# Kernel tuning notes

Hardware: AMD Instinct MI355X
Metric: run time of the kernel (lower is better)

The kernel has to match this reference:

```python
import jax, jax.numpy as jnp
import numpy as np

B, S, D = 4, 2048, 1024
H, DH = 16, 64


def setup_inputs() -> dict:
    key = jax.random.key(0)
    ks = jax.random.split(key, 5)
    x = jax.random.normal(ks[0], (B, S, D), dtype=jnp.float32)
    # causal mask: True where attention is disallowed (j > i)
    mask = jnp.triu(jnp.ones((S, S), dtype=bool), k=1)
    mask = jnp.broadcast_to(mask, (B, S, S))
    scale = 1.0 / np.sqrt(D)
    w_q = jax.random.normal(ks[1], (D, D), dtype=jnp.float32) * scale
    w_k = jax.random.normal(ks[2], (D, D), dtype=jnp.float32) * scale
    w_v = jax.random.normal(ks[3], (D, D), dtype=jnp.float32) * scale
    w_o = jax.random.normal(ks[4], (D, D), dtype=jnp.float32) * scale
    return {"x": x, "mask": mask, "w_q": w_q, "w_k": w_k, "w_v": w_v, "w_o": w_o}


def reference(x, mask, w_q, w_k, w_v, w_o):
    # torch Linear: y = x @ W.T (bias=False)
    b, s, d = x.shape
    q = (x @ w_q.T).reshape(b, s, H, DH).transpose(0, 2, 1, 3)  # [B,H,S,DH]
    k = (x @ w_k.T).reshape(b, s, H, DH).transpose(0, 2, 1, 3)
    v = (x @ w_v.T).reshape(b, s, H, DH).transpose(0, 2, 1, 3)
    inv_sqrt_dh = jnp.asarray(1.0 / np.sqrt(DH), dtype=x.dtype)
    scores = jnp.einsum('bhqd,bhkd->bhqk', q * inv_sqrt_dh, k)  # [B,H,S,S]
    scores = jnp.where(mask[:, None, :, :], -jnp.inf, scores)
    attn = jax.nn.softmax(scores, axis=-1)  # dropout is identity in eval mode
    out = jnp.einsum('bhqk,bhkd->bhqd', attn, v)  # [B,H,S,DH]
    out = out.transpose(0, 2, 1, 3).reshape(b, s, d)
    out = out @ w_o.T
    return out, attn
```

## Files before the change

kernel.cpp:

```cpp
#include <hip/hip_runtime.h>

#define DEV __device__ __forceinline__

typedef __attribute__((ext_vector_type(8))) short short8;
typedef __attribute__((ext_vector_type(4))) float f32x4;

DEV unsigned short f2bf(float f) {
  unsigned u = __builtin_bit_cast(unsigned, f);
  u += 0x7fff + ((u >> 16) & 1);
  return (unsigned short)(u >> 16);
}

DEV void gload_lds16(const void* g, void* l) {
  __builtin_amdgcn_global_load_lds(
      (const __attribute__((address_space(1))) void*)g,
      (__attribute__((address_space(3))) void*)l, 16, 0, 0);
}

#if __has_builtin(__builtin_amdgcn_exp2f)
#define EXP2F(x) __builtin_amdgcn_exp2f(x)
#else
#define EXP2F(x) exp2f(x)
#endif

#define LOG2E 1.4426950408889634f
#define QSCALE (0.125f * LOG2E)
#define MFMA16(a, b, c) __builtin_amdgcn_mfma_f32_16x16x32_bf16((a), (b), (c), 0, 0, 0)

__global__ void cvt_f32_bf16(const float* __restrict__ in, unsigned short* __restrict__ out, int n4) {
  int i = blockIdx.x * blockDim.x + threadIdx.x;
  int stride = gridDim.x * blockDim.x;
  for (; i < n4; i += stride) {
    float4 v = ((const float4*)in)[i];
    ushort4 o;
    o.x = f2bf(v.x); o.y = f2bf(v.y); o.z = f2bf(v.z); o.w = f2bf(v.w);
    ((ushort4*)out)[i] = o;
  }
}

__global__ void cvt_w4(const float* __restrict__ w0, const float* __restrict__ w1,
                       const float* __restrict__ w2, const float* __restrict__ w3,
                       unsigned short* __restrict__ o0, unsigned short* __restrict__ o1,
                       unsigned short* __restrict__ o2, unsigned short* __restrict__ o3) {
  int i = blockIdx.x * blockDim.x + threadIdx.x;
  int sel = i >> 18, j = i & 0x3ffff;
  const float* in = sel == 0 ? w0 : sel == 1 ? w1 : sel == 2 ? w2 : w3;
  unsigned short* out = sel == 0 ? o0 : sel == 1 ? o1 : sel == 2 ? o2 : o3;
  float4 v = ((const float4*)in)[j];
  ushort4 o;
  o.x = f2bf(v.x); o.y = f2bf(v.y); o.z = f2bf(v.z); o.w = f2bf(v.w);
  ((ushort4*)out)[j] = o;
}

#define GK 1024
template <int MODE>
DEV void gemm_body(const unsigned short* A, const unsigned short* Bw, void* Cout,
                   int bx, int by) {
  __shared__ unsigned short Ash[128 * 32];
  __shared__ unsigned short Bsh[128 * 32];
  const int tid = threadIdx.x;
  const int lane = tid & 63;
  const int w = tid >> 6;
  const int wm = w >> 1, wn = w & 1;
  const int l15 = lane & 15, l4 = lane >> 4;
  const int row0 = by * 128;
  const int col0 = bx * 128;

  f32x4 acc[4][4] = {};

  for (int kt = 0; kt < GK; kt += 32) {
    __syncthreads();
#pragma unroll
    for (int c = 0; c < 2; ++c) {
      int o = c * 4096 + tid * 16;
      int ldsoff = c * 4096 + w * 1024;
      int row = o >> 6, colb = o & 63;
      gload_lds16((const char*)A + (size_t)(row0 + row) * 2048 + kt * 2 + colb,
                  (char*)Ash + ldsoff);
      gload_lds16((const char*)Bw + (size_t)(col0 + row) * 2048 + kt * 2 + colb,
                  (char*)Bsh + ldsoff);
    }
    __syncthreads();
    short8 af[4], bf[4];
#pragma unroll
    for (int m = 0; m < 4; ++m)
      af[m] = *(const short8*)((const char*)Ash + (wm * 64 + m * 16 + l15) * 64 + l4 * 16);
#pragma unroll
    for (int n = 0; n < 4; ++n)
      bf[n] = *(const short8*)((const char*)Bsh + (wn * 64 + n * 16 + l15) * 64 + l4 * 16);
#pragma unroll
    for (int m = 0; m < 4; ++m)
#pragma unroll
      for (int n = 0; n < 4; ++n)
        acc[m][n] = MFMA16(af[m], bf[n], acc[m][n]);
  }

#pragma unroll
  for (int m = 0; m < 4; ++m)
#pragma unroll
    for (int n = 0; n < 4; ++n)
#pragma unroll
      for (int r = 0; r < 4; ++r) {
        int mrow = row0 + wm * 64 + m * 16 + l4 * 4 + r;
        int ncol = col0 + wn * 64 + n * 16 + l15;
        float v = acc[m][n][r];
        if (MODE == 0) {
          ((unsigned short*)Cout)[(size_t)mrow * 1024 + ncol] = f2bf(v);
        } else if (MODE == 1) {
          int b = mrow >> 11, s = mrow & 2047, h = ncol >> 6, d = ncol & 63;
          ((unsigned short*)Cout)[((size_t)((b * 16 + h) * 64 + d)) * 2048 + s] = f2bf(v);
        } else if (MODE == 2) {
          ((float*)Cout)[(size_t)mrow * 1024 + ncol] = v;
        } else {
          ((unsigned short*)Cout)[(size_t)mrow * 1024 + ncol] = f2bf(v * QSCALE);
        }
      }
}

__global__ __launch_bounds__(256) void gemm_qkv(const unsigned short* __restrict__ A,
                                                const unsigned short* __restrict__ Wq,
                                                const unsigned short* __restrict__ Wk,
                                                const unsigned short* __restrict__ Wv,
                                                unsigned short* __restrict__ Qo,
                                                unsigned short* __restrict__ Ko,
                                                unsigned short* __restrict__ Vto) {
  const int z = blockIdx.z;
  if (z == 0)      gemm_body<3>(A, Wq, Qo,  blockIdx.x, blockIdx.y);
  else if (z == 1) gemm_body<0>(A, Wk, Ko,  blockIdx.x, blockIdx.y);
  else             gemm_body<1>(A, Wv, Vto, blockIdx.x, blockIdx.y);
}

__global__ __launch_bounds__(256) void gemm_out(const unsigned short* __restrict__ A,
                                                const unsigned short* __restrict__ Bw,
                                                float* __restrict__ Cout) {
  gemm_body<2>(A, Bw, Cout, blockIdx.x, blockIdx.y);
}


DEV void stage_tile(const unsigned short* src_base, size_t row_stride, int col0,
                    char* ldsbase, int tid) {
  const int w = tid >> 6;
  const int r0 = tid >> 3;
  const int c0 = (tid & 7) ^ (r0 & 7);
  gload_lds16((const char*)(src_base + (size_t)r0 * row_stride + col0 + c0 * 8),
              ldsbase + w * 1024);
  const int r1 = 32 + r0;
  gload_lds16((const char*)(src_base + (size_t)r1 * row_stride + col0 + c0 * 8),
              ldsbase + 4096 + w * 1024);
}

__global__ __launch_bounds__(256, 4) void attn_fused(const unsigned short* __restrict__ Q,
                                                     const unsigned short* __restrict__ Kb,
                                                     const unsigned short* __restrict__ Vt,
                                                     float* __restrict__ attn,
                                                     unsigned short* __restrict__ O) {
  __shared__ char lds[40960];

  const int tid = threadIdx.x, lane = tid & 63, w = tid >> 6;
  const int l15 = lane & 15, l4 = lane >> 4;
  const int s7 = l15 & 7;
  const int off0 = (l4 ^ s7) << 4;
  const int off1 = ((l4 + 4) ^ s7) << 4;
  const int F = blockIdx.x;
  const int xcd = F & 7, slot = F >> 3;
  const int pr = slot & 15;
  const int bh = xcd + ((slot >> 4) << 3);
  const int b = bh >> 4, h = bh & 15;

  const size_t qk_base = ((size_t)b * 2048) * 1024 + h * 64;
  const unsigned short* Qp = Q + qk_base;
  const unsigned short* Kp = Kb + qk_base;
  const unsigned short* Vp = Vt + (size_t)bh * 64 * 2048;
  float* Ap = attn + (size_t)bh * 2048 * 2048;
  char* pbase = lds + 32768 + w * 2048;

  for (int t = 0; t < 2; ++t) {
    const int qt = t ? (31 - pr) : pr;
    const int q0 = qt * 64 + w * 16;
    const int myq = q0 + l15;

    short8 qf[2];
    {
      const char* qrow = (const char*)(Qp + (size_t)(q0 + l15) * 1024);
      qf[0] = *(const short8*)(qrow + (l4 * 8) * 2);
      qf[1] = *(const short8*)(qrow + (32 + l4 * 8) * 2);
    }

    float lacc[4] = {0.f, 0.f, 0.f, 0.f};
    {
      stage_tile(Kp, 1024, 0, lds, tid);
      if (qt >= 1) stage_tile(Kp + (size_t)64 * 1024, 1024, 0, lds + 8192, tid);
      __syncthreads();
      const int nst = (qt + 2) >> 1;
      for (int st = 0; st < nst; ++st) {
        char* kbb = lds + (st & 1) * 16384;
        const int jt0 = 2 * st;
        if (jt0 + 2 <= qt) {
          char* nb = lds + ((st + 1) & 1) * 16384;
          stage_tile(Kp + (size_t)(jt0 + 2) * 64 * 1024, 1024, 0, nb, tid);
          if (jt0 + 3 <= qt)
            stage_tile(Kp + (size_t)(jt0 + 3) * 64 * 1024, 1024, 0, nb + 8192, tid);
        }
#pragma unroll
        for (int u = 0; u < 2; ++u) {
          const int jt = jt0 + u;
          if (jt > qt) break;
          const char* kb = kbb + u * 8192;
          const int jbase = jt * 64;
          const bool diag = (jt == qt);
#pragma unroll
          for (int jb = 0; jb < 4; ++jb) {
            const char* krow = kb + (jb * 16 + l15) * 128;
            short8 k0 = *(const short8*)(krow + off0);
            short8 k1 = *(const short8*)(krow + off1);
            f32x4 a = {};
            a = MFMA16(k0, qf[0], a);
            a = MFMA16(k1, qf[1], a);
#pragma unroll
            for (int r = 0; r < 4; ++r) {
              int j = jbase + jb * 16 + l4 * 4 + r;
              float e = EXP2F(a[r]);
              lacc[r] += (diag && j > myq) ? 0.f : e;
            }
          }
        }
        __syncthreads();
      }
    }
    float lsum = (lacc[0] + lacc[1]) + (lacc[2] + lacc[3]);
    lsum += __shfl_xor(lsum, 16);
    lsum += __shfl_xor(lsum, 32);
    const float inv_l = 1.f / lsum;

    f32x4 oacc[4] = {};
    stage_tile(Kp, 1024, 0, lds, tid);
    stage_tile(Vp, 2048, 0, lds + 16384, tid);
    __syncthreads();
    for (int jt = 0; jt <= qt; ++jt) {
      const char* kb = lds + (jt & 1) * 8192;
      const char* vb = lds + 16384 + (jt & 1) * 8192;
      if (jt < qt) {
        stage_tile(Kp + (size_t)(jt + 1) * 64 * 1024, 1024, 0,
                   lds + ((jt + 1) & 1) * 8192, tid);
        stage_tile(Vp, 2048, (jt + 1) * 64, lds + 16384 + ((jt + 1) & 1) * 8192, tid);
      }
      const int jbase = jt * 64;
      const bool diag = (jt == qt);
      float p[16];
#pragma unroll
      for (int jb = 0; jb < 4; ++jb) {
        const char* krow = kb + (jb * 16 + l15) * 128;
        short8 k0 = *(const short8*)(krow + off0);
        short8 k1 = *(const short8*)(krow + off1);
        f32x4 a = {};
        a = MFMA16(k0, qf[0], a);
        a = MFMA16(k1, qf[1], a);
#pragma unroll
        for (int r = 0; r < 4; ++r) {
          int j = jbase + jb * 16 + l4 * 4 + r;
          float e = EXP2F(a[r]) * inv_l;
          p[jb * 4 + r] = (diag && j > myq) ? 0.f : e;
        }
      }
#pragma unroll
      for (int jb = 0; jb < 4; ++jb) {
        f32x4 pv = {p[jb * 4], p[jb * 4 + 1], p[jb * 4 + 2], p[jb * 4 + 3]};
        *(f32x4*)(Ap + (size_t)myq * 2048 + jbase + jb * 16 + l4 * 4) = pv;
      }
#pragma unroll
      for (int jb = 0; jb < 4; ++jb) {
        unsigned u0 = f2bf(p[jb * 4]) | ((unsigned)f2bf(p[jb * 4 + 1]) << 16);
        unsigned u1 = f2bf(p[jb * 4 + 2]) | ((unsigned)f2bf(p[jb * 4 + 3]) << 16);
        uint2 uu; uu.x = u0; uu.y = u1;
        *(uint2*)(pbase + (jb * 2 + (l4 >> 1)) * 256 + l15 * 16 + (l4 & 1) * 8) = uu;
      }
      short8 pa0 = *(const short8*)(pbase + l4 * 256 + l15 * 16);
      short8 pa1 = *(const short8*)(pbase + (4 + l4) * 256 + l15 * 16);
#pragma unroll
      for (int db = 0; db < 4; ++db) {
        const char* vrow = vb + (db * 16 + l15) * 128;
        short8 v0 = *(const short8*)(vrow + off0);
        short8 v1 = *(const short8*)(vrow + off1);
        oacc[db] = MFMA16(pa0, v0, oacc[db]);
        oacc[db] = MFMA16(pa1, v1, oacc[db]);
      }
      __syncthreads();
    }

    for (int jt = qt + 1; jt < 32; ++jt) {
      const int jbase = jt * 64;
      f32x4 z = {};
#pragma unroll
      for (int jb = 0; jb < 4; ++jb)
        *(f32x4*)(Ap + (size_t)myq * 2048 + jbase + jb * 16 + l4 * 4) = z;
    }

#pragma unroll
    for (int db = 0; db < 4; ++db)
#pragma unroll
      for (int r = 0; r < 4; ++r) {
        int q = q0 + l4 * 4 + r;
        int d = db * 16 + l15;
        O[((size_t)b * 2048 + q) * 1024 + h * 64 + d] = f2bf(oacc[db][r]);
      }
  }
}

extern "C" void kernel_launch(void* const* d_in, const int* in_sizes, int n_in,
                              void* d_out, int out_size, void* d_ws, size_t ws_size,
                              hipStream_t stream) {
  const float* x  = (const float*)d_in[0];
  const float* wq = (const float*)d_in[2];
  const float* wk = (const float*)d_in[3];
  const float* wv = (const float*)d_in[4];
  const float* wo = (const float*)d_in[5];

  float* out  = (float*)d_out;
  float* attn = out + (size_t)8192 * 1024;

  char* ws = (char*)d_ws;
  const size_t MB = 1 << 20;
  unsigned short* xb  = (unsigned short*)(ws);
  unsigned short* wqb = (unsigned short*)(ws + 16 * MB);
  unsigned short* wkb = (unsigned short*)(ws + 18 * MB);
  unsigned short* wvb = (unsigned short*)(ws + 20 * MB);
  unsigned short* wob = (unsigned short*)(ws + 22 * MB);
  unsigned short* Qb  = (unsigned short*)(ws + 24 * MB);
  unsigned short* Kb  = (unsigned short*)(ws + 40 * MB);
  unsigned short* Vtb = (unsigned short*)(ws + 56 * MB);
  unsigned short* Ob  = (unsigned short*)(ws + 72 * MB);

  cvt_f32_bf16<<<2048, 256, 0, stream>>>(x, xb, 8192 * 1024 / 4);
  cvt_w4<<<4096, 256, 0, stream>>>(wq, wk, wv, wo, wqb, wkb, wvb, wob);

  gemm_qkv<<<dim3(8, 64, 3), 256, 0, stream>>>(xb, wqb, wkb, wvb, Qb, Kb, Vtb);

  attn_fused<<<1024, 256, 0, stream>>>(Qb, Kb, Vtb, attn, Ob);

  gemm_out<<<dim3(8, 64), 256, 0, stream>>>(Ob, wob, out);
}
```

Baseline: 446.7 us.

## Process both paired query tiles together, sharing K/V LDS staging

The attention kernel now handles its two causally paired query tiles (pr and 31-pr) in one pass over the keys instead of two sequential passes. Each K and V tile staged into LDS serves both query tiles, which removes the duplicate K/V loads and barriers for the shorter tile. The block-to-tile mapping also alternates pr order across groups to balance work. The cost is roughly doubled register state (two sets of Q fragments, row sums and output accumulators), which may hurt occupancy or cause spills under launch_bounds(256,4).

```diff
diff --git a/kernel.cpp b/kernel.cpp
--- a/kernel.cpp
+++ b/kernel.cpp
@@ -149,6 +149,49 @@
               ldsbase + 4096 + w * 1024);
 }
 
+DEV void tile_B(const char* kb, const char* vb, char* pbase,
+                const short8* qf, float inv_l, int jbase, bool diag, int myq,
+                float* Arow, f32x4* oacc, int l15, int l4, int off0, int off1) {
+  float p[16];
+#pragma unroll
+  for (int jb = 0; jb < 4; ++jb) {
+    const char* krow = kb + (jb * 16 + l15) * 128;
+    short8 k0 = *(const short8*)(krow + off0);
+    short8 k1 = *(const short8*)(krow + off1);
+    f32x4 a = {};
+    a = MFMA16(k0, qf[0], a);
+    a = MFMA16(k1, qf[1], a);
+#pragma unroll
+    for (int r = 0; r < 4; ++r) {
+      int j = jbase + jb * 16 + l4 * 4 + r;
+      float e = EXP2F(a[r]) * inv_l;
+      p[jb * 4 + r] = (diag && j > myq) ? 0.f : e;
+    }
+  }
+#pragma unroll
+  for (int jb = 0; jb < 4; ++jb) {
+    f32x4 pv = {p[jb * 4], p[jb * 4 + 1], p[jb * 4 + 2], p[jb * 4 + 3]};
+    *(f32x4*)(Arow + jbase + jb * 16 + l4 * 4) = pv;
+  }
+#pragma unroll
+  for (int jb = 0; jb < 4; ++jb) {
+    unsigned u0 = f2bf(p[jb * 4]) | ((unsigned)f2bf(p[jb * 4 + 1]) << 16);
+    unsigned u1 = f2bf(p[jb * 4 + 2]) | ((unsigned)f2bf(p[jb * 4 + 3]) << 16);
+    uint2 uu; uu.x = u0; uu.y = u1;
+    *(uint2*)(pbase + (jb * 2 + (l4 >> 1)) * 256 + l15 * 16 + (l4 & 1) * 8) = uu;
+  }
+  short8 pa0 = *(const short8*)(pbase + l4 * 256 + l15 * 16);
+  short8 pa1 = *(const short8*)(pbase + (4 + l4) * 256 + l15 * 16);
+#pragma unroll
+  for (int db = 0; db < 4; ++db) {
+    const char* vrow = vb + (db * 16 + l15) * 128;
+    short8 v0 = *(const short8*)(vrow + off0);
+    short8 v1 = *(const short8*)(vrow + off1);
+    oacc[db] = MFMA16(pa0, v0, oacc[db]);
+    oacc[db] = MFMA16(pa1, v1, oacc[db]);
+  }
+}
+
 __global__ __launch_bounds__(256, 4) void attn_fused(const unsigned short* __restrict__ Q,
                                                      const unsigned short* __restrict__ Kb,
                                                      const unsigned short* __restrict__ Vt,
@@ -163,9 +206,14 @@
   const int off1 = ((l4 + 4) ^ s7) << 4;
   const int F = blockIdx.x;
   const int xcd = F & 7, slot = F >> 3;
-  const int pr = slot & 15;
-  const int bh = xcd + ((slot >> 4) << 3);
+  const int g = slot >> 4, r = slot & 15;
+  const int pr = ((g >> 1) & 1) ? (15 - r) : r;
+  const int bh = xcd + (g << 3);
   const int b = bh >> 4, h = bh & 15;
+
+  const int qt0 = pr, qt1 = 31 - pr;
+  const int q00 = qt0 * 64 + w * 16, q01 = qt1 * 64 + w * 16;
+  const int myq0 = q00 + l15, myq1 = q01 + l15;
 
   const size_t qk_base = ((size_t)b * 2048) * 1024 + h * 64;
   const unsigned short* Qp = Q + qk_base;
@@ -174,136 +222,130 @@
   float* Ap = attn + (size_t)bh * 2048 * 2048;
   char* pbase = lds + 32768 + w * 2048;
 
-  for (int t = 0; t < 2; ++t) {
-    const int qt = t ? (31 - pr) : pr;
-    const int q0 = qt * 64 + w * 16;
-    const int myq = q0 + l15;
-
-    short8 qf[2];
-    {
-      const char* qrow = (const char*)(Qp + (size_t)(q0 + l15) * 1024);
-      qf[0] = *(const short8*)(qrow + (l4 * 8) * 2);
-      qf[1] = *(const short8*)(qrow + (32 + l4 * 8) * 2);
-    }
-
-    float lacc[4] = {0.f, 0.f, 0.f, 0.f};
-    {
-      stage_tile(Kp, 1024, 0, lds, tid);
-      if (qt >= 1) stage_tile(Kp + (size_t)64 * 1024, 1024, 0, lds + 8192, tid);
-      __syncthreads();
-      const int nst = (qt + 2) >> 1;
-      for (int st = 0; st < nst; ++st) {
-        char* kbb = lds + (st & 1) * 16384;
-        const int jt0 = 2 * st;
-        if (jt0 + 2 <= qt) {
-          char* nb = lds + ((st + 1) & 1) * 16384;
-          stage_tile(Kp + (size_t)(jt0 + 2) * 64 * 1024, 1024, 0, nb, tid);
-          if (jt0 + 3 <= qt)
-            stage_tile(Kp + (size_t)(jt0 + 3) * 64 * 1024, 1024, 0, nb + 8192, tid);
-        }
-#pragma unroll
-        for (int u = 0; u < 2; ++u) {
-          const int jt = jt0 + u;
-          if (jt > qt) break;
-          const char* kb = kbb + u * 8192;
-          const int jbase = jt * 64;
-          const bool diag = (jt == qt);
-#pragma unroll
-          for (int jb = 0; jb < 4; ++jb) {
-            const char* krow = kb + (jb * 16 + l15) * 128;
-            short8 k0 = *(const short8*)(krow + off0);
-            short8 k1 = *(const short8*)(krow + off1);
-            f32x4 a = {};
-            a = MFMA16(k0, qf[0], a);
-            a = MFMA16(k1, qf[1], a);
-#pragma unroll
-            for (int r = 0; r < 4; ++r) {
-              int j = jbase + jb * 16 + l4 * 4 + r;
-              float e = EXP2F(a[r]);
-              lacc[r] += (diag && j > myq) ? 0.f : e;
+  short8 qf0[2], qf1[2];
+  {
+    const char* qrow0 = (const char*)(Qp + (size_t)myq0 * 1024);
+    qf0[0] = *(const short8*)(qrow0 + (l4 * 8) * 2);
+    qf0[1] = *(const short8*)(qrow0 + (32 + l4 * 8) * 2);
+    const char* qrow1 = (const char*)(Qp + (size_t)myq1 * 1024);
+    qf1[0] = *(const short8*)(qrow1 + (l4 * 8) * 2);
+    qf1[1] = *(const short8*)(qrow1 + (32 + l4 * 8) * 2);
+  }
+
+  float lacc0[4] = {0.f, 0.f, 0.f, 0.f};
+  float lacc1[4] = {0.f, 0.f, 0.f, 0.f};
+  {
+    stage_tile(Kp, 1024, 0, lds, tid);
+    stage_tile(Kp + (size_t)64 * 1024, 1024, 0, lds + 8192, tid);
+    __syncthreads();
+    const int nst = (qt1 + 2) >> 1;
+    for (int st = 0; st < nst; ++st) {
+      char* kbb = lds + (st & 1) * 16384;
+      const int jt0 = 2 * st;
+      if (jt0 + 2 <= qt1) {
+        char* nb = lds + ((st + 1) & 1) * 16384;
+        stage_tile(Kp + (size_t)(jt0 + 2) * 64 * 1024, 1024, 0, nb, tid);
+        if (jt0 + 3 <= qt1)
+          stage_tile(Kp + (size_t)(jt0 + 3) * 64 * 1024, 1024, 0, nb + 8192, tid);
+      }
+#pragma unroll
+      for (int u = 0; u < 2; ++u) {
+        const int jt = jt0 + u;
+        if (jt > qt1) break;
+        const char* kb = kbb + u * 8192;
+        const int jbase = jt * 64;
+        const bool diag1 = (jt == qt1);
+        const bool do0 = (jt <= qt0);
+        const bool diag0 = (jt == qt0);
+#pragma unroll
+        for (int jb = 0; jb < 4; ++jb) {
+          const char* krow = kb + (jb * 16 + l15) * 128;
+          short8 k0 = *(const short8*)(krow + off0);
+          short8 k1 = *(const short8*)(krow + off1);
+          f32x4 a1 = {};
+          a1 = MFMA16(k0, qf1[0], a1);
+          a1 = MFMA16(k1, qf1[1], a1);
+#pragma unroll
+          for (int rr = 0; rr < 4; ++rr) {
+            int j = jbase + jb * 16 + l4 * 4 + rr;
+            float e = EXP2F(a1[rr]);
+            lacc1[rr] += (diag1 && j > myq1) ? 0.f : e;
+          }
+          if (do0) {
+            f32x4 a0 = {};
+            a0 = MFMA16(k0, qf0[0], a0);
+            a0 = MFMA16(k1, qf0[1], a0);
+#pragma unroll
+            for (int rr = 0; rr < 4; ++rr) {
+              int j = jbase + jb * 16 + l4 * 4 + rr;
+              float e = EXP2F(a0[rr]);
+              lacc0[rr] += (diag0 && j > myq0) ? 0.f : e;
             }
           }
         }
-        __syncthreads();
-      }
-    }
-    float lsum = (lacc[0] + lacc[1]) + (lacc[2] + lacc[3]);
-    lsum += __shfl_xor(lsum, 16);
-    lsum += __shfl_xor(lsum, 32);
-    const float inv_l = 1.f / lsum;
-
-    f32x4 oacc[4] = {};
-    stage_tile(Kp, 1024, 0, lds, tid);
-    stage_tile(Vp, 2048, 0, lds + 16384, tid);
-    __syncthreads();
-    for (int jt = 0; jt <= qt; ++jt) {
-      const char* kb = lds + (jt & 1) * 8192;
-      const char* vb = lds + 16384 + (jt & 1) * 8192;
-      if (jt < qt) {
-        stage_tile(Kp + (size_t)(jt + 1) * 64 * 1024, 1024, 0,
-                   lds + ((jt + 1) & 1) * 8192, tid);
-        stage_tile(Vp, 2048, (jt + 1) * 64, lds + 16384 + ((jt + 1) & 1) * 8192, tid);
-      }
-      const int jbase = jt * 64;
-      const bool diag = (jt == qt);
-      float p[16];
-#pragma unroll
-      for (int jb = 0; jb < 4; ++jb) {
-        const char* krow = kb + (jb * 16 + l15) * 128;
-        short8 k0 = *(const short8*)(krow + off0);
-        short8 k1 = *(const short8*)(krow + off1);
-        f32x4 a = {};
-        a = MFMA16(k0, qf[0], a);
-        a = MFMA16(k1, qf[1], a);
-#pragma unroll
-        for (int r = 0; r < 4; ++r) {
-          int j = jbase + jb * 16 + l4 * 4 + r;
-          float e = EXP2F(a[r]) * inv_l;
-          p[jb * 4 + r] = (diag && j > myq) ? 0.f : e;
-        }
-      }
-#pragma unroll
-      for (int jb = 0; jb < 4; ++jb) {
-        f32x4 pv = {p[jb * 4], p[jb * 4 + 1], p[jb * 4 + 2], p[jb * 4 + 3]};
-        *(f32x4*)(Ap + (size_t)myq * 2048 + jbase + jb * 16 + l4 * 4) = pv;
-      }
-#pragma unroll
-      for (int jb = 0; jb < 4; ++jb) {
-        unsigned u0 = f2bf(p[jb * 4]) | ((unsigned)f2bf(p[jb * 4 + 1]) << 16);
-        unsigned u1 = f2bf(p[jb * 4 + 2]) | ((unsigned)f2bf(p[jb * 4 + 3]) << 16);
-        uint2 uu; uu.x = u0; uu.y = u1;
-        *(uint2*)(pbase + (jb * 2 + (l4 >> 1)) * 256 + l15 * 16 + (l4 & 1) * 8) = uu;
-      }
-      short8 pa0 = *(const short8*)(pbase + l4 * 256 + l15 * 16);
-      short8 pa1 = *(const short8*)(pbase + (4 + l4) * 256 + l15 * 16);
-#pragma unroll
-      for (int db = 0; db < 4; ++db) {
-        const char* vrow = vb + (db * 16 + l15) * 128;
-        short8 v0 = *(const short8*)(vrow + off0);
-        short8 v1 = *(const short8*)(vrow + off1);
-        oacc[db] = MFMA16(pa0, v0, oacc[db]);
-        oacc[db] = MFMA16(pa1, v1, oacc[db]);
       }
       __syncthreads();
     }
-
-    for (int jt = qt + 1; jt < 32; ++jt) {
+  }
+  float lsum0 = (lacc0[0] + lacc0[1]) + (lacc0[2] + lacc0[3]);
+  lsum0 += __shfl_xor(lsum0, 16);
+  lsum0 += __shfl_xor(lsum0, 32);
+  float lsum1 = (lacc1[0] + lacc1[1]) + (lacc1[2] + lacc1[3]);
+  lsum1 += __shfl_xor(lsum1, 16);
+  lsum1 += __shfl_xor(lsum1, 32);
+  const float inv_l0 = 1.f / lsum0;
+  const float inv_l1 = 1.f / lsum1;
+
+  f32x4 oacc0[4] = {};
+  f32x4 oacc1[4] = {};
+  float* Arow0 = Ap + (size_t)myq0 * 2048;
+  float* Arow1 = Ap + (size_t)myq1 * 2048;
+  stage_tile(Kp, 1024, 0, lds, tid);
+  stage_tile(Vp, 2048, 0, lds + 16384, tid);
+  __syncthreads();
+  for (int jt = 0; jt <= qt1; ++jt) {
+    const char* kb = lds + (jt & 1) * 8192;
+    const char* vb = lds + 16384 + (jt & 1) * 8192;
+    if (jt < qt1) {
+      stage_tile(Kp + (size_t)(jt + 1) * 64 * 1024, 1024, 0,
+                 lds + ((jt + 1) & 1) * 8192, tid);
+      stage_tile(Vp, 2048, (jt + 1) * 64, lds + 16384 + ((jt + 1) & 1) * 8192, tid);
+    }
+    const int jbase = jt * 64;
+    tile_B(kb, vb, pbase, qf1, inv_l1, jbase, jt == qt1, myq1, Arow1, oacc1,
+           l15, l4, off0, off1);
+    if (jt <= qt0)
+      tile_B(kb, vb, pbase, qf0, inv_l0, jbase, jt == qt0, myq0, Arow0, oacc0,
+             l15, l4, off0, off1);
+    __syncthreads();
+  }
+
+  {
+    f32x4 z = {};
+    for (int jt = qt0 + 1; jt < 32; ++jt) {
       const int jbase = jt * 64;
-      f32x4 z = {};
 #pragma unroll
       for (int jb = 0; jb < 4; ++jb)
-        *(f32x4*)(Ap + (size_t)myq * 2048 + jbase + jb * 16 + l4 * 4) = z;
-    }
-
-#pragma unroll
-    for (int db = 0; db < 4; ++db)
-#pragma unroll
-      for (int r = 0; r < 4; ++r) {
-        int q = q0 + l4 * 4 + r;
-        int d = db * 16 + l15;
-        O[((size_t)b * 2048 + q) * 1024 + h * 64 + d] = f2bf(oacc[db][r]);
-      }
-  }
+        *(f32x4*)(Arow0 + jbase + jb * 16 + l4 * 4) = z;
+    }
+    for (int jt = qt1 + 1; jt < 32; ++jt) {
+      const int jbase = jt * 64;
+#pragma unroll
+      for (int jb = 0; jb < 4; ++jb)
+        *(f32x4*)(Arow1 + jbase + jb * 16 + l4 * 4) = z;
+    }
+  }
+
+#pragma unroll
+  for (int db = 0; db < 4; ++db)
+#pragma unroll
+    for (int rr = 0; rr < 4; ++rr) {
+      int d = db * 16 + l15;
+      int qa = q00 + l4 * 4 + rr;
+      O[((size_t)b * 2048 + qa) * 1024 + h * 64 + d] = f2bf(oacc0[db][rr]);
+      int qb2 = q01 + l4 * 4 + rr;
+      O[((size_t)b * 2048 + qb2) * 1024 + h * 64 + d] = f2bf(oacc1[db][rr]);
+    }
 }
 
 extern "C" void kernel_launch(void* const* d_in, const int* in_sizes, int n_in,
```

After: 575.7 us. 1.29x slower.
